# Kernel tuning notes

Measured on AMD Instinct MI355X. Metric: run time of the kernel, lower is better.

Reference implementation:

```python
import jax, jax.numpy as jnp
import numpy as np
import math

B, T, C = 32, 256, 1024
LAYER_ID, NUM_LAYERS = 12, 24
NEG_INF = -1e38


def setup_inputs() -> dict:
    key = jax.random.key(0)
    ks = jax.random.split(key, 5)
    x = jax.random.normal(ks[0], (B, T, C), dtype=jnp.float32)
    # deterministic parameter init, faithful to the torch __init__
    r01 = LAYER_ID / (NUM_LAYERS - 1)          # ratio_0_to_1
    r10 = 1.0 - LAYER_ID / NUM_LAYERS          # ratio_1_to_almost0
    h = jnp.arange(C, dtype=jnp.float32)
    time_decay = -5.0 + 8.0 * (h / (C - 1)) ** (0.7 + 1.3 * r01)
    tf = (jnp.arange(C) + 1) % 3 - 1
    time_first = jnp.full((C,), math.log(0.3), jnp.float32) + 0.5 * tf.astype(jnp.float32)
    xr = (jnp.arange(C, dtype=jnp.float32) / C)[None, None, :]   # [1,1,C]
    time_mix_k = xr ** r10
    time_mix_v = xr ** r10 + 0.3 * r01
    time_mix_r = xr ** (0.5 * r10)
    s = 1.0 / math.sqrt(C)
    Wk = jax.random.normal(ks[1], (C, C), jnp.float32) * s
    Wv = jax.random.normal(ks[2], (C, C), jnp.float32) * s
    Wr = jax.random.normal(ks[3], (C, C), jnp.float32) * s
    Wo = jax.random.normal(ks[4], (C, C), jnp.float32) * s
    return {"x": x, "time_decay": time_decay, "time_first": time_first,
            "time_mix_k": time_mix_k, "time_mix_v": time_mix_v, "time_mix_r": time_mix_r,
            "Wk": Wk, "Wv": Wv, "Wr": Wr, "Wo": Wo}


def wkv(time_decay, time_first, k, v):
    """Numerically-stabilized WKV scan. k,v: [B,T,C]; decay/first: [C]."""
    w = -jnp.exp(time_decay)   # per-channel log-decay (negative)
    u = time_first
    kT = jnp.swapaxes(k, 0, 1)  # [T,B,C]
    vT = jnp.swapaxes(v, 0, 1)

    def step(carry, kv):
        p, q, o = carry                       # p,q: running num/den; o: log scale
        kt, vt = kv                           # [B,C]
        no = jnp.maximum(o, u + kt)
        A = jnp.exp(o - no)
        Bc = jnp.exp(u + kt - no)
        y = (A * p + Bc * vt) / (A * q + Bc)
        no2 = jnp.maximum(w + o, kt)
        A2 = jnp.exp(w + o - no2)
        B2 = jnp.exp(kt - no2)
        return (A2 * p + B2 * vt, A2 * q + B2, no2), y

    init = (jnp.zeros((k.shape[0], k.shape[2]), k.dtype),
            jnp.zeros((k.shape[0], k.shape[2]), k.dtype),
            jnp.full((k.shape[0], k.shape[2]), NEG_INF, k.dtype))
    _, yT = jax.lax.scan(step, init, (kT, vT))
    return jnp.swapaxes(yT, 0, 1)  # [B,T,C]


def reference(x, time_decay, time_first, time_mix_k, time_mix_v, time_mix_r, Wk, Wv, Wr, Wo):
    # time_shift: xx[t] = x[t-1], xx[0] = 0
    xx = jnp.pad(x, ((0, 0), (1, 0), (0, 0)))[:, :-1, :]
    xk = x * time_mix_k + xx * (1.0 - time_mix_k)
    xv = x * time_mix_v + xx * (1.0 - time_mix_v)
    xr = x * time_mix_r + xx * (1.0 - time_mix_r)
    k = jnp.einsum('btc,dc->btd', xk, Wk)
    v = jnp.einsum('btc,dc->btd', xv, Wv)
    r = jnp.einsum('btc,dc->btd', xr, Wr)
    sr = jax.nn.sigmoid(r)
    rwkv = sr * wkv(time_decay, time_first, k, v)
    return jnp.einsum('btc,dc->btd', rwkv, Wo)
```

## Files before the change

kernel.cpp:

```cpp
#include <hip/hip_runtime.h>

#define Bdim 32
#define Tdim 256
#define Cdim 1024

typedef unsigned short u16;
typedef unsigned int u32;
typedef __bf16 bf16x8 __attribute__((ext_vector_type(8)));
typedef float f32x4 __attribute__((ext_vector_type(4)));

__device__ __forceinline__ float bf2f(u32 u) {
    union { u32 i; float f; } v; v.i = u << 16; return v.f;
}
__device__ __forceinline__ u16 f2bf(float f) {
    union { float f; u32 i; } v; v.f = f;
    u32 u = v.i;
    return (u16)((u + 0x7fffu + ((u >> 16) & 1u)) >> 16);
}

__device__ __forceinline__ void gload16(const u16* g, u16* l) {
    __builtin_amdgcn_global_load_lds(
        (__attribute__((address_space(1))) const void*)g,
        (__attribute__((address_space(3))) void*)l, 16, 0, 0);
}

__global__ __launch_bounds__(256) void prep_fused(
    const float* __restrict__ x, const float* __restrict__ tmk,
    const float* __restrict__ tmv, const float* __restrict__ tmr,
    u16* __restrict__ xk, u16* __restrict__ xv, u16* __restrict__ xr,
    const float* __restrict__ w0, const float* __restrict__ w1,
    const float* __restrict__ w2, const float* __restrict__ w3,
    u16* __restrict__ o0, u16* __restrict__ o1,
    u16* __restrict__ o2, u16* __restrict__ o3)
{
    int bid = blockIdx.x;
    if (bid < 4096) {
        int tid = bid * 256 + threadIdx.x;
        int e = tid << 3;
        int c = e & (Cdim - 1);
        int t = (e >> 10) & (Tdim - 1);
        float xf[8], xxf[8], mk[8], mv[8], mr[8];
        *(float4*)(xf)     = *(const float4*)(x + e);
        *(float4*)(xf + 4) = *(const float4*)(x + e + 4);
        if (t != 0) {
            *(float4*)(xxf)     = *(const float4*)(x + e - Cdim);
            *(float4*)(xxf + 4) = *(const float4*)(x + e - Cdim + 4);
        } else {
#pragma unroll
            for (int j = 0; j < 8; j++) xxf[j] = 0.f;
        }
        *(float4*)(mk)     = *(const float4*)(tmk + c);
        *(float4*)(mk + 4) = *(const float4*)(tmk + c + 4);
        *(float4*)(mv)     = *(const float4*)(tmv + c);
        *(float4*)(mv + 4) = *(const float4*)(tmv + c + 4);
        *(float4*)(mr)     = *(const float4*)(tmr + c);
        *(float4*)(mr + 4) = *(const float4*)(tmr + c + 4);
        u16 ok[8], ov[8], orr[8];
#pragma unroll
        for (int j = 0; j < 8; j++) {
            float d = xf[j] - xxf[j];
            ok[j]  = f2bf(xxf[j] + d * mk[j]);
            ov[j]  = f2bf(xxf[j] + d * mv[j]);
            orr[j] = f2bf(xxf[j] + d * mr[j]);
        }
        *(uint4*)(xk + e) = *(const uint4*)ok;
        *(uint4*)(xv + e) = *(const uint4*)ov;
        *(uint4*)(xr + e) = *(const uint4*)orr;
    } else {
        int wb = bid - 4096;
        int m = wb >> 9;
        const float* src; u16* dst;
        switch (m) {
            case 0: src = w0; dst = o0; break;
            case 1: src = w1; dst = o1; break;
            case 2: src = w2; dst = o2; break;
            default: src = w3; dst = o3; break;
        }
        int i = (((wb & 511) << 8) + threadIdx.x) << 3;
        float a[8];
        *(float4*)(a)     = *(const float4*)(src + i);
        *(float4*)(a + 4) = *(const float4*)(src + i + 4);
        u16 o[8];
#pragma unroll
        for (int j = 0; j < 8; j++) o[j] = f2bf(a[j]);
        *(uint4*)(dst + i) = *(const uint4*)o;
    }
}

template <int BF16OUT>
__device__ __forceinline__ void gemm_body256(
    const u16* __restrict__ A, const u16* __restrict__ Bw, void* __restrict__ Cout,
    u16* As, u16* Bs, int bm, int bn)
{
    const int K = Cdim, N = Cdim;
    const int NT = K / 64;
    const int tid = threadIdx.x;
    const int lane = tid & 63, wave = tid >> 6;
    const int wm = (wave >> 1) << 6;
    const int wn = (wave & 1) << 6;
    const int fr = lane & 15, quad = lane >> 4;
    const int lwo = wave << 9;

    const int srow = tid >> 3;
    const int schunk = ((tid & 7) ^ (srow & 7)) << 3;
    const u16* gaS = A  + (size_t)(bm * 256 + srow) * K + schunk;
    const u16* gbS = Bw + (size_t)(bn * 128 + srow) * K + schunk;
    const size_t rstep = (size_t)64 * K;

    const int koff0 = ((quad << 3))      ^ ((fr & 7) << 3);
    const int koff1 = (32 + (quad << 3)) ^ ((fr & 7) << 3);

    f32x4 acc[4][4];
#pragma unroll
    for (int i = 0; i < 4; i++)
#pragma unroll
        for (int j = 0; j < 4; j++)
            acc[i][j] = (f32x4){0.f, 0.f, 0.f, 0.f};

    auto issue2 = [&](int T, int aoff, int boff) {
        const u16* ga = gaS + T * 64;
        u16* la = As + aoff + lwo;
        gload16(ga,             la);
        gload16(ga + rstep,     la + 4096);
        gload16(ga + 2 * rstep, la + 8192);
        gload16(ga + 3 * rstep, la + 12288);
        const u16* gb = gbS + T * 64;
        u16* lb = Bs + boff + lwo;
        gload16(gb,         lb);
        gload16(gb + rstep, lb + 4096);
    };

    auto compute_tile = [&](int ac, int bc) {
        const u16* __restrict__ Ab = As + ac;
        const u16* __restrict__ Bb = Bs + bc;
        __builtin_amdgcn_s_setprio(1);
#pragma unroll
        for (int ph = 0; ph < 4; ++ph) {
            const int qi = ph >> 1, qj = ph & 1;
            bf16x8 af[2][2], bfr[2][2];
#pragma unroll
            for (int d = 0; d < 2; ++d) {
                const int ra = (wm + (qi * 2 + d) * 16 + fr) << 6;
                af[d][0] = *(const bf16x8*)(Ab + ra + koff0);
                af[d][1] = *(const bf16x8*)(Ab + ra + koff1);
                const int rb = (wn + (qj * 2 + d) * 16 + fr) << 6;
                bfr[d][0] = *(const bf16x8*)(Bb + rb + koff0);
                bfr[d][1] = *(const bf16x8*)(Bb + rb + koff1);
            }
#pragma unroll
            for (int di = 0; di < 2; ++di)
#pragma unroll
                for (int dj = 0; dj < 2; ++dj) {
                    acc[qi * 2 + di][qj * 2 + dj] =
                        __builtin_amdgcn_mfma_f32_16x16x32_bf16(
                            af[di][0], bfr[dj][0], acc[qi * 2 + di][qj * 2 + dj], 0, 0, 0);
                    acc[qi * 2 + di][qj * 2 + dj] =
                        __builtin_amdgcn_mfma_f32_16x16x32_bf16(
                            af[di][1], bfr[dj][1], acc[qi * 2 + di][qj * 2 + dj], 0, 0, 0);
                }
        }
        __builtin_amdgcn_s_setprio(0);
    };

    issue2(0, 0, 0);
    issue2(1, 16384, 8192);
    asm volatile("s_waitcnt vmcnt(6)" ::: "memory");
    __builtin_amdgcn_s_barrier();
    __builtin_amdgcn_sched_barrier(0);

    int a_c = 0, b_c = 0;
    int a_s = 32768, b_s = 16384;
#pragma unroll 1
    for (int t = 0; t <= NT - 3; ++t) {
        issue2(t + 2, a_s, b_s);
        compute_tile(a_c, b_c);
        asm volatile("s_waitcnt vmcnt(6)" ::: "memory");
        __builtin_amdgcn_s_barrier();
        __builtin_amdgcn_sched_barrier(0);
        a_c += 16384; if (a_c == 49152) a_c = 0;
        b_c += 8192;  if (b_c == 24576) b_c = 0;
        a_s += 16384; if (a_s == 49152) a_s = 0;
        b_s += 8192;  if (b_s == 24576) b_s = 0;
    }
    compute_tile(a_c, b_c);
    asm volatile("s_waitcnt vmcnt(0)" ::: "memory");
    __builtin_amdgcn_s_barrier();
    __builtin_amdgcn_sched_barrier(0);
    a_c += 16384; if (a_c == 49152) a_c = 0;
    b_c += 8192;  if (b_c == 24576) b_c = 0;
    compute_tile(a_c, b_c);

    const int gr0 = bm * 256 + wm + quad * 4;
    const int gc0 = bn * 128 + wn + fr;
#pragma unroll
    for (int i = 0; i < 4; i++)
#pragma unroll
        for (int j = 0; j < 4; j++)
#pragma unroll
            for (int r = 0; r < 4; r++) {
                int gr = gr0 + i * 16 + r;
                int gc = gc0 + j * 16;
                float val = acc[i][j][r];
                if (BF16OUT)
                    ((u16*)Cout)[(size_t)gr * N + gc] = f2bf(val);
                else
                    ((float*)Cout)[(size_t)gr * N + gc] = val;
            }
}

__global__ __launch_bounds__(512) void gemm3_kernel(
    const u16* __restrict__ xk, const u16* __restrict__ xv, const u16* __restrict__ xr,
    const u16* __restrict__ wk, const u16* __restrict__ wv, const u16* __restrict__ wr,
    u16* __restrict__ ck, u16* __restrict__ cv, u16* __restrict__ cr)
{
    __shared__ __align__(16) u16 As[3 * 16384];
    __shared__ __align__(16) u16 Bs[3 * 8192];
    const u16* A; const u16* Bw; u16* Cout;
    switch (blockIdx.z) {
        case 0:  A = xk; Bw = wk; Cout = ck; break;
        case 1:  A = xv; Bw = wv; Cout = cv; break;
        default: A = xr; Bw = wr; Cout = cr; break;
    }
    int bx = blockIdx.x;
    gemm_body256<1>(A, Bw, (void*)Cout, As, Bs, bx & 31, bx >> 5);
}

__global__ __launch_bounds__(512) void gemmo_kernel(
    const u16* __restrict__ A, const u16* __restrict__ Bw, float* __restrict__ Cout)
{
    __shared__ __align__(16) u16 As[3 * 16384];
    __shared__ __align__(16) u16 Bs[3 * 8192];
    int bx = blockIdx.x;
    gemm_body256<0>(A, Bw, (void*)Cout, As, Bs, bx & 31, bx >> 5);
}

#define WTC 16

#define LOADCHUNK(KA, VA, RA, T0)                                        \
    _Pragma("unroll")                                                    \
    for (int s = 0; s < WTC; s++) {                                      \
        size_t idx = base + (size_t)((T0) + s) * Cdim;                   \
        KA[s] = kb[idx]; VA[s] = vb[idx]; RA[s] = rb[idx];               \
    }

#define COMPCHUNK(KA, VA, RA, T0)                                        \
    _Pragma("unroll")                                                    \
    for (int s = 0; s < WTC; s++) {                                      \
        float kt = bf2f(KA[s]);                                          \
        float vt = bf2f(VA[s]);                                          \
        float rt = bf2f(RA[s]);                                          \
        float uk = u + kt;                                               \
        float no = fmaxf(o, uk);                                         \
        float Ae = __expf(o - no);                                       \
        float Bc = __expf(uk - no);                                      \
        float num = Ae * p + Bc * vt;                                    \
        float den = Ae * q + Bc;                                         \
        float y = num * __builtin_amdgcn_rcpf(den);                      \
        float sr = __builtin_amdgcn_rcpf(1.f + __expf(-rt));             \
        rwkv[base + (size_t)((T0) + s) * Cdim] = f2bf(y * sr);           \
        float wo = w + o;                                                \
        float no2 = fmaxf(wo, kt);                                       \
        float A2 = __expf(wo - no2);                                     \
        float B2 = __expf(kt - no2);                                     \
        p = A2 * p + B2 * vt;                                            \
        q = A2 * q + B2;                                                 \
        o = no2;                                                         \
    }

__global__ __launch_bounds__(64) void wkv_kernel(
    const u16* __restrict__ kb, const u16* __restrict__ vb,
    const u16* __restrict__ rb, const float* __restrict__ td,
    const float* __restrict__ tfirst, u16* __restrict__ rwkv)
{
    int lane = threadIdx.x;
    int blk = blockIdx.x;
    int b = blk >> 4;
    int c = ((blk & 15) << 6) + lane;
    float w = -__expf(td[c]);
    float u = tfirst[c];
    const size_t base = (size_t)b * Tdim * Cdim + c;

    u32 kA[WTC], vA[WTC], rA[WTC];
    u32 kB[WTC], vB[WTC], rB[WTC];
    float p = 0.f, q = 0.f, o = -1e38f;

    LOADCHUNK(kA, vA, rA, 0)
    for (int t0 = 0; t0 < Tdim; t0 += 2 * WTC) {
        LOADCHUNK(kB, vB, rB, t0 + WTC)
        COMPCHUNK(kA, vA, rA, t0)
        if (t0 + 2 * WTC < Tdim) {
            LOADCHUNK(kA, vA, rA, t0 + 2 * WTC)
        }
        COMPCHUNK(kB, vB, rB, t0 + WTC)
    }
}

extern "C" void kernel_launch(void* const* d_in, const int* in_sizes, int n_in,
                              void* d_out, int out_size, void* d_ws, size_t ws_size,
                              hipStream_t stream) {
    (void)in_sizes; (void)n_in; (void)out_size; (void)ws_size;
    const float* x   = (const float*)d_in[0];
    const float* td  = (const float*)d_in[1];
    const float* tfi = (const float*)d_in[2];
    const float* tmk = (const float*)d_in[3];
    const float* tmv = (const float*)d_in[4];
    const float* tmr = (const float*)d_in[5];
    const float* Wk  = (const float*)d_in[6];
    const float* Wv  = (const float*)d_in[7];
    const float* Wr  = (const float*)d_in[8];
    const float* Wo  = (const float*)d_in[9];

    char* ws = (char*)d_ws;
    const size_t MiB = (size_t)1 << 20;
    u16* xk    = (u16*)(ws);
    u16* xv    = (u16*)(ws + 16 * MiB);
    u16* xr    = (u16*)(ws + 32 * MiB);
    u16* wkb   = (u16*)(ws + 48 * MiB);
    u16* wvb   = (u16*)(ws + 50 * MiB);
    u16* wrb   = (u16*)(ws + 52 * MiB);
    u16* wob   = (u16*)(ws + 54 * MiB);
    u16* kb    = (u16*)(ws + 56 * MiB);
    u16* vb    = (u16*)(ws + 72 * MiB);
    u16* rb    = (u16*)(ws + 88 * MiB);
    u16* rwkvb = (u16*)(ws);

    prep_fused<<<6144, 256, 0, stream>>>(x, tmk, tmv, tmr, xk, xv, xr,
                                         Wk, Wv, Wr, Wo, wkb, wvb, wrb, wob);

    gemm3_kernel<<<dim3(256, 1, 3), 512, 0, stream>>>(xk, xv, xr, wkb, wvb, wrb,
                                                      kb, vb, rb);

    wkv_kernel<<<512, 64, 0, stream>>>(kb, vb, rb, td, tfi, rwkvb);

    gemmo_kernel<<<256, 512, 0, stream>>>(rwkvb, wob, (float*)d_out);
}
```

Before: 243.7 us.

## Split GEMM main loop into two k-halves interleaving LDS reads, loads and MFMA

Restructures the GEMM inner loop so each 64-wide k tile is processed in two halves. Each half loads all A/B fragments from LDS, issues part of the next global-to-LDS prefetch, then runs a 16-MFMA burst between barriers. The goal is to interleave global load issue with MFMA work, ping-pong style, and to cut register pressure by holding only half the fragments at a time. It adds more barriers per iteration and folds the epilogue iterations into the loop with conditional waits.

```diff
diff --git a/kernel.cpp b/kernel.cpp
--- a/kernel.cpp
+++ b/kernel.cpp
@@ -107,8 +107,10 @@
     const u16* gbS = Bw + (size_t)(bn * 128 + srow) * K + schunk;
     const size_t rstep = (size_t)64 * K;
 
-    const int koff0 = ((quad << 3))      ^ ((fr & 7) << 3);
-    const int koff1 = (32 + (quad << 3)) ^ ((fr & 7) << 3);
+    const int koff0 = (((0 + quad) ^ (fr & 7)) << 3);
+    const int koff1 = (((4 + quad) ^ (fr & 7)) << 3);
+    const int arow = wm + fr;
+    const int brow = wn + fr;
 
     f32x4 acc[4][4];
 #pragma unroll
@@ -117,78 +119,85 @@
         for (int j = 0; j < 4; j++)
             acc[i][j] = (f32x4){0.f, 0.f, 0.f, 0.f};
 
-    auto issue2 = [&](int T, int aoff, int boff) {
+    auto issueA3 = [&](int T, int aoff) {
         const u16* ga = gaS + T * 64;
         u16* la = As + aoff + lwo;
         gload16(ga,             la);
         gload16(ga + rstep,     la + 4096);
         gload16(ga + 2 * rstep, la + 8192);
-        gload16(ga + 3 * rstep, la + 12288);
+    };
+    auto issueA1B2 = [&](int T, int aoff, int boff) {
+        const u16* ga = gaS + T * 64;
+        gload16(ga + 3 * rstep, As + aoff + lwo + 12288);
         const u16* gb = gbS + T * 64;
         u16* lb = Bs + boff + lwo;
         gload16(gb,         lb);
         gload16(gb + rstep, lb + 4096);
     };
 
-    auto compute_tile = [&](int ac, int bc) {
-        const u16* __restrict__ Ab = As + ac;
-        const u16* __restrict__ Bb = Bs + bc;
-        __builtin_amdgcn_s_setprio(1);
-#pragma unroll
-        for (int ph = 0; ph < 4; ++ph) {
-            const int qi = ph >> 1, qj = ph & 1;
-            bf16x8 af[2][2], bfr[2][2];
-#pragma unroll
-            for (int d = 0; d < 2; ++d) {
-                const int ra = (wm + (qi * 2 + d) * 16 + fr) << 6;
-                af[d][0] = *(const bf16x8*)(Ab + ra + koff0);
-                af[d][1] = *(const bf16x8*)(Ab + ra + koff1);
-                const int rb = (wn + (qj * 2 + d) * 16 + fr) << 6;
-                bfr[d][0] = *(const bf16x8*)(Bb + rb + koff0);
-                bfr[d][1] = *(const bf16x8*)(Bb + rb + koff1);
-            }
-#pragma unroll
-            for (int di = 0; di < 2; ++di)
-#pragma unroll
-                for (int dj = 0; dj < 2; ++dj) {
-                    acc[qi * 2 + di][qj * 2 + dj] =
-                        __builtin_amdgcn_mfma_f32_16x16x32_bf16(
-                            af[di][0], bfr[dj][0], acc[qi * 2 + di][qj * 2 + dj], 0, 0, 0);
-                    acc[qi * 2 + di][qj * 2 + dj] =
-                        __builtin_amdgcn_mfma_f32_16x16x32_bf16(
-                            af[di][1], bfr[dj][1], acc[qi * 2 + di][qj * 2 + dj], 0, 0, 0);
-                }
-        }
-        __builtin_amdgcn_s_setprio(0);
-    };
-
-    issue2(0, 0, 0);
-    issue2(1, 16384, 8192);
+#define MFMA16(AR, BR)                                                   \
+    _Pragma("unroll")                                                    \
+    for (int i = 0; i < 4; ++i)                                          \
+        _Pragma("unroll")                                                \
+        for (int j = 0; j < 4; ++j)                                      \
+            acc[i][j] = __builtin_amdgcn_mfma_f32_16x16x32_bf16(         \
+                AR[i], BR[j], acc[i][j], 0, 0, 0);
+
+    issueA3(0, 0);
+    issueA1B2(0, 0, 0);
+    issueA3(1, 16384);
+    issueA1B2(1, 16384, 8192);
     asm volatile("s_waitcnt vmcnt(6)" ::: "memory");
     __builtin_amdgcn_s_barrier();
-    __builtin_amdgcn_sched_barrier(0);
 
     int a_c = 0, b_c = 0;
     int a_s = 32768, b_s = 16384;
 #pragma unroll 1
-    for (int t = 0; t <= NT - 3; ++t) {
-        issue2(t + 2, a_s, b_s);
-        compute_tile(a_c, b_c);
-        asm volatile("s_waitcnt vmcnt(6)" ::: "memory");
+    for (int t = 0; t < NT; ++t) {
+        const u16* __restrict__ Ab = As + a_c;
+        const u16* __restrict__ Bb = Bs + b_c;
+        const bool st = (t + 2 < NT);
+        bf16x8 a[4], b[4];
+
+#pragma unroll
+        for (int i = 0; i < 4; ++i)
+            a[i] = *(const bf16x8*)(Ab + (arow + i * 16) * 64 + koff0);
+#pragma unroll
+        for (int j = 0; j < 4; ++j)
+            b[j] = *(const bf16x8*)(Bb + (brow + j * 16) * 64 + koff0);
+        if (st) issueA3(t + 2, a_s);
         __builtin_amdgcn_s_barrier();
-        __builtin_amdgcn_sched_barrier(0);
+        asm volatile("s_waitcnt lgkmcnt(0)" ::: "memory");
+        __builtin_amdgcn_s_setprio(1);
+        MFMA16(a, b)
+        __builtin_amdgcn_s_setprio(0);
+        __builtin_amdgcn_s_barrier();
+
+#pragma unroll
+        for (int i = 0; i < 4; ++i)
+            a[i] = *(const bf16x8*)(Ab + (arow + i * 16) * 64 + koff1);
+#pragma unroll
+        for (int j = 0; j < 4; ++j)
+            b[j] = *(const bf16x8*)(Bb + (brow + j * 16) * 64 + koff1);
+        if (st) issueA1B2(t + 2, a_s, b_s);
+        __builtin_amdgcn_s_barrier();
+        asm volatile("s_waitcnt lgkmcnt(0)" ::: "memory");
+        __builtin_amdgcn_s_setprio(1);
+        MFMA16(a, b)
+        __builtin_amdgcn_s_setprio(0);
+        if (st) {
+            asm volatile("s_waitcnt vmcnt(6)" ::: "memory");
+        } else if (t == NT - 2) {
+            asm volatile("s_waitcnt vmcnt(0)" ::: "memory");
+        }
+        __builtin_amdgcn_s_barrier();
+
         a_c += 16384; if (a_c == 49152) a_c = 0;
         b_c += 8192;  if (b_c == 24576) b_c = 0;
         a_s += 16384; if (a_s == 49152) a_s = 0;
         b_s += 8192;  if (b_s == 24576) b_s = 0;
     }
-    compute_tile(a_c, b_c);
-    asm volatile("s_waitcnt vmcnt(0)" ::: "memory");
-    __builtin_amdgcn_s_barrier();
-    __builtin_amdgcn_sched_barrier(0);
-    a_c += 16384; if (a_c == 49152) a_c = 0;
-    b_c += 8192;  if (b_c == 24576) b_c = 0;
-    compute_tile(a_c, b_c);
+#undef MFMA16
 
     const int gr0 = bm * 256 + wm + quad * 4;
     const int gc0 = bn * 128 + wn + fr;
```

New measurement: 229.3 us. -5.9%, faster.
